# Kernel optimization log

Hardware: AMD Instinct MI355X
Metric: run time of the kernel (lower is better)

Reference implementation:

```python
import jax, jax.numpy as jnp
import numpy as np

EPS = 1e-5
NEG = -9e15

def layer_norm(x, gamma, beta):
    mu = jnp.mean(x, axis=-1, keepdims=True)
    var = jnp.var(x, axis=-1, keepdims=True)
    return (x - mu) * jax.lax.rsqrt(var + EPS) * gamma + beta

def setup_inputs() -> dict:
    key = jax.random.key(0)
    ks = jax.random.split(key, 8)
    B, S, D, F = 4, 4096, 128, 512
    q = jax.random.normal(ks[0], (B, S, D), dtype=jnp.float32)
    k = jax.random.normal(ks[1], (B, S, D), dtype=jnp.float32)
    v = jax.random.normal(ks[2], (B, S, D), dtype=jnp.float32)
    w1 = jax.random.normal(ks[3], (D, F), dtype=jnp.float32) / np.sqrt(D)
    b1 = jnp.zeros((F,), dtype=jnp.float32)
    w2 = jax.random.normal(ks[4], (F, D), dtype=jnp.float32) / np.sqrt(F)
    b2 = jnp.zeros((D,), dtype=jnp.float32)
    g1 = jnp.ones((D,), dtype=jnp.float32)
    be1 = jnp.zeros((D,), dtype=jnp.float32)
    g2 = jnp.ones((D,), dtype=jnp.float32)
    be2 = jnp.zeros((D,), dtype=jnp.float32)
    return {"q": q, "k": k, "v": v, "w1": w1, "b1": b1, "w2": w2, "b2": b2,
            "g1": g1, "be1": be1, "g2": g2, "be2": be2}

def reference(q, k, v, w1, b1, w2, b2, g1, be1, g2, be2):
    d_k = q.shape[-1]
    # naive attention: [B,S,S] logits materialized, as in the original
    logits = jnp.einsum('bqd,bkd->bqk', q, k) / jnp.sqrt(jnp.asarray(d_k, q.dtype))
    attn = jax.nn.softmax(logits, axis=-1)
    attn_out = jnp.einsum('bqk,bkd->bqd', attn, v)
    x = layer_norm(attn_out, g1, be1)
    ffn = jnp.maximum(x @ w1 + b1, 0) @ w2 + b2
    return layer_norm(x + ffn, g2, be2)
```

## Files before the change

kernel.cpp:

```cpp
#include <hip/hip_runtime.h>
#include <hip/hip_bf16.h>

typedef __attribute__((ext_vector_type(8))) __bf16 bf16x8;
typedef __attribute__((ext_vector_type(4))) __bf16 bf16x4;
typedef __attribute__((ext_vector_type(4))) float f32x4;
typedef __attribute__((ext_vector_type(16))) float f32x16;

#define MFMA16(a, b, c) __builtin_amdgcn_mfma_f32_16x16x32_bf16((a), (b), (c), 0, 0, 0)
#define MFMA32(a, b, c) __builtin_amdgcn_mfma_f32_32x32x16_bf16((a), (b), (c), 0, 0, 0)

static constexpr int S_LEN = 4096;
static constexpr int DH = 128;
static constexpr int NR = 4 * S_LEN;
static constexpr float QSCALE = 0.12752551286084110f;

__device__ inline bf16x8 pack8(float4 a, float4 b) {
  bf16x8 r;
  r[0] = (__bf16)a.x; r[1] = (__bf16)a.y; r[2] = (__bf16)a.z; r[3] = (__bf16)a.w;
  r[4] = (__bf16)b.x; r[5] = (__bf16)b.y; r[6] = (__bf16)b.z; r[7] = (__bf16)b.w;
  return r;
}

__device__ __forceinline__ float fexp2(float x) {
#if __has_builtin(__builtin_amdgcn_exp2f)
  return __builtin_amdgcn_exp2f(x);
#else
  return exp2f(x);
#endif
}

__device__ __forceinline__ unsigned packbf(float a, float b) {
  union { __bf16 h[2]; unsigned u; } t;
  t.h[0] = (__bf16)a;
  t.h[1] = (__bf16)b;
  return t.u;
}

typedef __attribute__((address_space(1))) const unsigned GU32;
typedef __attribute__((address_space(3))) unsigned LU32;
__device__ __forceinline__ void gl16(const void* g, void* s) {
  __builtin_amdgcn_global_load_lds((GU32*)g, (LU32*)s, 16, 0, 0);
}

__global__ __launch_bounds__(256) void prep_all(
    const float* __restrict__ K, const float* __restrict__ V,
    const float* __restrict__ Q, const float* __restrict__ w1,
    const float* __restrict__ w2, __bf16* __restrict__ Kb,
    __bf16* __restrict__ VTb, __bf16* __restrict__ Qb,
    __bf16* __restrict__ w1t, __bf16* __restrict__ w2t) {
  __shared__ float tile[32][33];
  const int bid = blockIdx.x;
  const int t = threadIdx.x;
  if (bid < 1024) {
    size_t i = ((size_t)bid * 256 + t) * 8;
    float4 a = *(const float4*)(K + i), b = *(const float4*)(K + i + 4);
    *(bf16x8*)(Kb + i) = pack8(a, b);
  } else if (bid < 3072) {
    const int bid2 = bid - 1024;
    const int b = bid2 >> 9, rem = bid2 & 511;
    const int s0 = (rem >> 2) * 32, d0 = (rem & 3) * 32;
    {
      int r = t >> 3, q = t & 7;
      float4 f = *(const float4*)(V + ((size_t)(b * S_LEN + s0 + r)) * DH + d0 + q * 4);
      tile[r][q * 4 + 0] = f.x; tile[r][q * 4 + 1] = f.y;
      tile[r][q * 4 + 2] = f.z; tile[r][q * 4 + 3] = f.w;
    }
    __syncthreads();
    {
      int dr = t >> 3, c2 = t & 7;
      bf16x4 u;
#pragma unroll
      for (int j = 0; j < 4; ++j) u[j] = (__bf16)tile[c2 * 4 + j][dr];
      int c2s = (c2 & 4) | ((c2 & 1) << 1) | ((c2 >> 1) & 1);
      *(bf16x4*)(VTb + ((size_t)(b * DH + d0 + dr)) * S_LEN + s0 + c2s * 4) = u;
    }
  } else if (bid < 4096) {
    size_t i = ((size_t)(bid - 3072) * 256 + t) * 8;
    float4 a = *(const float4*)(Q + i), b = *(const float4*)(Q + i + 4);
    a.x *= QSCALE; a.y *= QSCALE; a.z *= QSCALE; a.w *= QSCALE;
    b.x *= QSCALE; b.y *= QSCALE; b.z *= QSCALE; b.w *= QSCALE;
    *(bf16x8*)(Qb + i) = pack8(a, b);
  } else {
    int i = (bid - 4096) * 256 + t;
    {
      int n = i >> 7, kk = i & 127;
      w1t[i] = (__bf16)w1[kk * 512 + n];
    }
    {
      int n = i >> 9, kk = i & 511;
      w2t[i] = (__bf16)w2[kk * 128 + n];
    }
  }
}

template <int NSP>
__global__ __launch_bounds__(256, 2) void attn_fa(
    const __bf16* __restrict__ Qb, const __bf16* __restrict__ Kb,
    const __bf16* __restrict__ VTb, __bf16* __restrict__ Op,
    float* __restrict__ lbuf) {
  constexpr int NTT = (S_LEN / NSP) / 64;
  __shared__ __attribute__((aligned(16))) __bf16 kl[2][64 * 128];
  __shared__ __attribute__((aligned(16))) __bf16 vt[2][128 * 64];

  const int tid = threadIdx.x;
  const int w = tid >> 6, l = tid & 63;
  const int q5 = l & 31, hi = l >> 5;
  const int bid = blockIdx.x;
  const int split = bid % NSP;
  const int qt = (bid / NSP) % 32;
  const int b = bid / (NSP * 32);
  const int R = b * S_LEN + qt * 128 + w * 32 + q5;
  const int kv0 = split * (S_LEN / NSP);

  bf16x8 qf[8];
  {
    const __bf16* qp = Qb + (size_t)R * DH + hi * 8;
#pragma unroll
    for (int kc = 0; kc < 8; ++kc) qf[kc] = *(const bf16x8*)(qp + kc * 16);
  }

  f32x16 o[4];
#pragma unroll
  for (int db = 0; db < 4; ++db) o[db] = f32x16{};
  float lsum = 0.f;

  const __bf16* kbase = Kb + (size_t)b * S_LEN * DH;
  const __bf16* vbase = VTb + (size_t)b * DH * S_LEN;

#define STAGE(BUF, S_OFF)                                                      \
  {                                                                            \
    _Pragma("unroll") for (int i = 0; i < 4; ++i) {                            \
      int r = w * 16 + i * 4 + (l >> 4);                                       \
      gl16(kbase + (size_t)((S_OFF) + r) * DH + (((l & 15) * 8) ^ ((r & 7) << 3)), \
           &kl[BUF][(w * 16 + i * 4) * 128]);                                  \
    }                                                                          \
    _Pragma("unroll") for (int i = 0; i < 4; ++i) {                            \
      int d = w * 32 + i * 8 + (l >> 3);                                       \
      gl16(vbase + (size_t)d * S_LEN + (S_OFF) + (((l & 7) * 8) ^ ((d & 7) << 3)), \
           &vt[BUF][(w * 32 + i * 8) * 64]);                                   \
    }                                                                          \
  }

  STAGE(0, kv0);
  __syncthreads();

  const int swz = (q5 & 7) << 3;

  int cur = 0;
  for (int t = 0; t < NTT; ++t) {
    if (t + 1 < NTT) STAGE(cur ^ 1, kv0 + (t + 1) * 64);

    bf16x8 pb[4];
#pragma unroll
    for (int kvb = 0; kvb < 2; ++kvb) {
      f32x16 acc = f32x16{};
      const int row = kvb * 32 + q5;
#pragma unroll
      for (int kc = 0; kc < 8; ++kc) {
        bf16x8 kf = *(const bf16x8*)&kl[cur][(row * 128 + kc * 16 + hi * 8) ^ swz];
        acc = MFMA32(kf, qf[kc], acc);
      }
      unsigned pk[4][2];
#pragma unroll
      for (int t4 = 0; t4 < 4; ++t4) {
        float e0 = fexp2(acc[4 * t4 + 0]), e1 = fexp2(acc[4 * t4 + 1]);
        float e2 = fexp2(acc[4 * t4 + 2]), e3 = fexp2(acc[4 * t4 + 3]);
        lsum += (e0 + e1) + (e2 + e3);
        pk[t4][0] = packbf(e0, e1);
        pk[t4][1] = packbf(e2, e3);
      }
#pragma unroll
      for (int kc2 = 0; kc2 < 2; ++kc2) {
        union { unsigned u[4]; bf16x8 v; } uu;
        uu.u[0] = pk[2 * kc2][0];
        uu.u[1] = pk[2 * kc2][1];
        uu.u[2] = pk[2 * kc2 + 1][0];
        uu.u[3] = pk[2 * kc2 + 1][1];
        pb[kvb * 2 + kc2] = uu.v;
      }
    }

#pragma unroll
    for (int db = 0; db < 4; ++db) {
      const int row = db * 32 + q5;
#pragma unroll
      for (int kc = 0; kc < 4; ++kc) {
        bf16x8 vf = *(const bf16x8*)&vt[cur][(row * 64 + kc * 16 + hi * 8) ^ swz];
        o[db] = MFMA32(vf, pb[kc], o[db]);
      }
    }

    __syncthreads();
    cur ^= 1;
  }
#undef STAGE

  lsum += __shfl_xor(lsum, 32);
  const float inv = 1.f / lsum;
  __bf16* orow = Op + ((size_t)split * NR + R) * DH;
#pragma unroll
  for (int db = 0; db < 4; ++db)
#pragma unroll
    for (int t4 = 0; t4 < 4; ++t4) {
      bf16x4 pk;
#pragma unroll
      for (int qi = 0; qi < 4; ++qi) pk[qi] = (__bf16)(o[db][4 * t4 + qi] * inv);
      *(bf16x4*)(orow + db * 32 + t4 * 8 + hi * 4) = pk;
    }
  if (hi == 0) lbuf[(size_t)split * NR + R] = lsum;
}

template <int NSP>
__global__ __launch_bounds__(256) void ffn_fused(
    const __bf16* __restrict__ Op, const float* __restrict__ lbuf,
    const float* __restrict__ g1, const float* __restrict__ be1,
    const __bf16* __restrict__ w1t, const __bf16* __restrict__ w2t,
    const float* __restrict__ b1, const float* __restrict__ b2,
    const float* __restrict__ g2, const float* __restrict__ be2,
    float* __restrict__ Out) {
  __shared__ __attribute__((aligned(16))) __bf16 xl[2][16 * 128];
  __shared__ float xr[2][16][132];
  __shared__ __attribute__((aligned(16))) __bf16 hl[16 * 512];
  __shared__ float part[4][16][2];

  const int tid = threadIdx.x;
  const int w = tid >> 6, l = tid & 63, lg = l >> 4, lc = l & 15;
  const int row0 = blockIdx.x * 32;

#pragma unroll
  for (int g = 0; g < 2; ++g) {
    const int prow = tid >> 4, pc8 = tid & 15;
    const int R = row0 + g * 16 + prow;
    float v[8] = {0.f, 0.f, 0.f, 0.f, 0.f, 0.f, 0.f, 0.f};
    float den = 0.f;
#pragma unroll
    for (int s = 0; s < NSP; ++s) {
      float ls = lbuf[(size_t)s * NR + R];
      den += ls;
      bf16x8 p = *(const bf16x8*)(Op + ((size_t)s * NR + R) * DH + pc8 * 8);
#pragma unroll
      for (int j = 0; j < 8; ++j) v[j] += ls * (float)p[j];
    }
    float inv = 1.f / den;
    float sm = 0.f, sq = 0.f;
#pragma unroll
    for (int j = 0; j < 8; ++j) {
      v[j] *= inv;
      sm += v[j];
      sq += v[j] * v[j];
    }
#pragma unroll
    for (int d = 1; d < 16; d <<= 1) {
      sm += __shfl_xor(sm, d);
      sq += __shfl_xor(sq, d);
    }
    float mu = sm * (1.f / 128.f);
    float var = sq * (1.f / 128.f) - mu * mu;
    float rs = rsqrtf(var + 1e-5f);
    float4 ga = *(const float4*)(g1 + pc8 * 8), gb = *(const float4*)(g1 + pc8 * 8 + 4);
    float4 ba = *(const float4*)(be1 + pc8 * 8), bb = *(const float4*)(be1 + pc8 * 8 + 4);
    float gv[8] = {ga.x, ga.y, ga.z, ga.w, gb.x, gb.y, gb.z, gb.w};
    float bv[8] = {ba.x, ba.y, ba.z, ba.w, bb.x, bb.y, bb.z, bb.w};
    bf16x8 xb;
    float xo[8];
#pragma unroll
    for (int j = 0; j < 8; ++j) {
      xo[j] = (v[j] - mu) * rs * gv[j] + bv[j];
      xb[j] = (__bf16)xo[j];
    }
    *(bf16x8*)&xl[g][(prow * 128 + pc8 * 8) ^ ((prow & 7) << 3)] = xb;
    *(float4*)&xr[g][prow][pc8 * 8] = make_float4(xo[0], xo[1], xo[2], xo[3]);
    *(float4*)&xr[g][prow][pc8 * 8 + 4] = make_float4(xo[4], xo[5], xo[6], xo[7]);
  }
  __syncthreads();

  for (int g = 0; g < 2; ++g) {
    bf16x8 xf[4];
    const int m = lc;
#pragma unroll
    for (int kc = 0; kc < 4; ++kc)
      xf[kc] = *(const bf16x8*)&xl[g][(m * 128 + kc * 32 + lg * 8) ^ ((m & 7) << 3)];

#pragma unroll
    for (int nb = 0; nb < 8; ++nb) {
      int n0 = w * 128 + nb * 16 + lc;
      const __bf16* wp = w1t + (size_t)n0 * 128 + lg * 8;
      f32x4 acc = (f32x4){0.f, 0.f, 0.f, 0.f};
#pragma unroll
      for (int kc = 0; kc < 4; ++kc)
        acc = MFMA16(xf[kc], *(const bf16x8*)(wp + kc * 32), acc);
      float bias = b1[n0];
#pragma unroll
      for (int r = 0; r < 4; ++r) {
        int rr = lg * 4 + r;
        hl[rr * 512 + (n0 ^ (lg << 4))] = (__bf16)fmaxf(acc[r] + bias, 0.f);
      }
    }
    __syncthreads();

    const int col0 = w * 32 + lc;
    f32x4 oo[2];
#pragma unroll
    for (int nb2 = 0; nb2 < 2; ++nb2) {
      int d0 = col0 + nb2 * 16;
      const __bf16* wp2 = w2t + (size_t)d0 * 512 + lg * 8;
      f32x4 acc = (f32x4){0.f, 0.f, 0.f, 0.f};
#pragma unroll
      for (int kc = 0; kc < 16; ++kc) {
        bf16x8 ha = *(const bf16x8*)&hl[lc * 512 + ((kc * 32 + lg * 8) ^ ((lc >> 2) << 4))];
        acc = MFMA16(ha, *(const bf16x8*)(wp2 + kc * 32), acc);
      }
      oo[nb2] = acc;
    }

    float b2v[2] = {b2[col0], b2[col0 + 16]};
    float g2v[2] = {g2[col0], g2[col0 + 16]};
    float be2v[2] = {be2[col0], be2[col0 + 16]};
    float sum[4] = {0.f, 0.f, 0.f, 0.f}, sq[4] = {0.f, 0.f, 0.f, 0.f};
#pragma unroll
    for (int nb2 = 0; nb2 < 2; ++nb2)
#pragma unroll
      for (int r = 0; r < 4; ++r) {
        int rr = lg * 4 + r;
        float xv = xr[g][rr][col0 + nb2 * 16];
        float tv = oo[nb2][r] + b2v[nb2] + xv;
        oo[nb2][r] = tv;
        sum[r] += tv;
        sq[r] += tv * tv;
      }
#pragma unroll
    for (int r = 0; r < 4; ++r) {
#pragma unroll
      for (int d = 1; d < 16; d <<= 1) {
        sum[r] += __shfl_xor(sum[r], d);
        sq[r] += __shfl_xor(sq[r], d);
      }
      if (lc == 0) {
        part[w][lg * 4 + r][0] = sum[r];
        part[w][lg * 4 + r][1] = sq[r];
      }
    }
    __syncthreads();

#pragma unroll
    for (int r = 0; r < 4; ++r) {
      int rr = lg * 4 + r;
      float S = 0.f, Qq = 0.f;
#pragma unroll
      for (int ww = 0; ww < 4; ++ww) {
        S += part[ww][rr][0];
        Qq += part[ww][rr][1];
      }
      float mu = S * (1.f / 128.f);
      float var = Qq * (1.f / 128.f) - mu * mu;
      float rs = rsqrtf(var + 1e-5f);
#pragma unroll
      for (int nb2 = 0; nb2 < 2; ++nb2)
        Out[(size_t)(row0 + g * 16 + rr) * DH + col0 + nb2 * 16] =
            (oo[nb2][r] - mu) * rs * g2v[nb2] + be2v[nb2];
    }
    __syncthreads();
  }
}

extern "C" void kernel_launch(void* const* d_in, const int* in_sizes, int n_in,
                              void* d_out, int out_size, void* d_ws, size_t ws_size,
                              hipStream_t stream) {
  const float* Q = (const float*)d_in[0];
  const float* K = (const float*)d_in[1];
  const float* V = (const float*)d_in[2];
  const float* w1 = (const float*)d_in[3];
  const float* b1 = (const float*)d_in[4];
  const float* w2 = (const float*)d_in[5];
  const float* b2 = (const float*)d_in[6];
  const float* g1 = (const float*)d_in[7];
  const float* be1 = (const float*)d_in[8];
  const float* g2 = (const float*)d_in[9];
  const float* be2 = (const float*)d_in[10];
  float* Out = (float*)d_out;

  char* p = (char*)d_ws;
  __bf16* w1t = (__bf16*)p;  p += 512 * 128 * 2;
  __bf16* w2t = (__bf16*)p;  p += 128 * 512 * 2;
  __bf16* Kb  = (__bf16*)p;  p += (size_t)NR * DH * 2;
  __bf16* VTb = (__bf16*)p;  p += (size_t)NR * DH * 2;
  __bf16* Qb  = (__bf16*)p;  p += (size_t)NR * DH * 2;
  float* lbuf = (float*)p;   p += (size_t)4 * NR * 4;
  __bf16* Op  = (__bf16*)p;

  prep_all<<<4352, 256, 0, stream>>>(K, V, Q, w1, w2, Kb, VTb, Qb, w1t, w2t);
  attn_fa<4><<<4 * 32 * 4, 256, 0, stream>>>(Qb, Kb, VTb, Op, lbuf);
  ffn_fused<4><<<NR / 32, 256, 0, stream>>>(Op, lbuf, g1, be1, w1t, w2t, b1,
                                            b2, g2, be2, Out);
}
```

Before: 86.48 us.

## Tile weight transposes through shared memory and raise wave priority around MFMA loops

```diff
diff --git a/kernel.cpp b/kernel.cpp
--- a/kernel.cpp
+++ b/kernel.cpp
@@ -81,14 +81,42 @@
     b.x *= QSCALE; b.y *= QSCALE; b.z *= QSCALE; b.w *= QSCALE;
     *(bf16x8*)(Qb + i) = pack8(a, b);
   } else {
-    int i = (bid - 4096) * 256 + t;
-    {
-      int n = i >> 7, kk = i & 127;
-      w1t[i] = (__bf16)w1[kk * 512 + n];
-    }
-    {
-      int n = i >> 9, kk = i & 511;
-      w2t[i] = (__bf16)w2[kk * 128 + n];
+    const int bw = bid - 4096;
+    if (bw < 64) {
+      const int tr = bw >> 4, tc = bw & 15;
+      const int r0 = tr * 32, c0 = tc * 32;
+      {
+        int row = t >> 3, q = t & 7;
+        float4 f = *(const float4*)(w1 + (size_t)(r0 + row) * 512 + c0 + q * 4);
+        tile[row][q * 4 + 0] = f.x; tile[row][q * 4 + 1] = f.y;
+        tile[row][q * 4 + 2] = f.z; tile[row][q * 4 + 3] = f.w;
+      }
+      __syncthreads();
+      {
+        int dr = t >> 3, c2 = t & 7;
+        bf16x4 u;
+#pragma unroll
+        for (int j = 0; j < 4; ++j) u[j] = (__bf16)tile[c2 * 4 + j][dr];
+        *(bf16x4*)(w1t + (size_t)(c0 + dr) * 128 + r0 + c2 * 4) = u;
+      }
+    } else {
+      const int bw2 = bw - 64;
+      const int tr = bw2 >> 2, tc = bw2 & 3;
+      const int r0 = tr * 32, c0 = tc * 32;
+      {
+        int row = t >> 3, q = t & 7;
+        float4 f = *(const float4*)(w2 + (size_t)(r0 + row) * 128 + c0 + q * 4);
+        tile[row][q * 4 + 0] = f.x; tile[row][q * 4 + 1] = f.y;
+        tile[row][q * 4 + 2] = f.z; tile[row][q * 4 + 3] = f.w;
+      }
+      __syncthreads();
+      {
+        int dr = t >> 3, c2 = t & 7;
+        bf16x4 u;
+#pragma unroll
+        for (int j = 0; j < 4; ++j) u[j] = (__bf16)tile[c2 * 4 + j][dr];
+        *(bf16x4*)(w2t + (size_t)(c0 + dr) * 512 + r0 + c2 * 4) = u;
+      }
     }
   }
 }
@@ -155,11 +183,13 @@
     for (int kvb = 0; kvb < 2; ++kvb) {
       f32x16 acc = f32x16{};
       const int row = kvb * 32 + q5;
+      __builtin_amdgcn_s_setprio(1);
 #pragma unroll
       for (int kc = 0; kc < 8; ++kc) {
         bf16x8 kf = *(const bf16x8*)&kl[cur][(row * 128 + kc * 16 + hi * 8) ^ swz];
         acc = MFMA32(kf, qf[kc], acc);
       }
+      __builtin_amdgcn_s_setprio(0);
       unsigned pk[4][2];
 #pragma unroll
       for (int t4 = 0; t4 < 4; ++t4) {
@@ -180,6 +210,7 @@
       }
     }
 
+    __builtin_amdgcn_s_setprio(1);
 #pragma unroll
     for (int db = 0; db < 4; ++db) {
       const int row = db * 32 + q5;
@@ -189,6 +220,7 @@
         o[db] = MFMA32(vf, pb[kc], o[db]);
       }
     }
+    __builtin_amdgcn_s_setprio(0);
 
     __syncthreads();
     cur ^= 1;
@@ -388,7 +420,7 @@
   float* lbuf = (float*)p;   p += (size_t)4 * NR * 4;
   __bf16* Op  = (__bf16*)p;
 
-  prep_all<<<4352, 256, 0, stream>>>(K, V, Q, w1, w2, Kb, VTb, Qb, w1t, w2t);
+  prep_all<<<4224, 256, 0, stream>>>(K, V, Q, w1, w2, Kb, VTb, Qb, w1t, w2t);
   attn_fa<4><<<4 * 32 * 4, 256, 0, stream>>>(Qb, Kb, VTb, Op, lbuf);
   ffn_fused<4><<<NR / 32, 256, 0, stream>>>(Op, lbuf, g1, be1, w1t, w2t, b1,
                                             b2, g2, be2, Out);
```

Result: no change. 86.27 us (-0.2%).
